# Optimization experiments

Measured on AMD Instinct MI355X. Metric: run time of the kernel, lower is better.

## Reference

```python
import jax, jax.numpy as jnp
import numpy as np

D, M, B, K = 512, 512, 8, 16
EPS = 1e-8
LAMBDA = 1.0
BALANCE_COEFF = 0.0


def _l2_normalize(x, axis=-1):
    n = jnp.linalg.norm(x, axis=axis, keepdims=True)
    return x / jnp.maximum(n, EPS)


def setup_inputs() -> dict:
    key = jax.random.key(0)
    k1, k2, k3 = jax.random.split(key, 3)
    x = jax.random.normal(k1, (2, 2048, D), dtype=jnp.float32)
    V = jax.random.normal(k2, (D, M, B), dtype=jnp.float32)
    U = jax.random.normal(k3, (M, D + 1, B), dtype=jnp.float32)
    return {"x": x, "V": V, "U": U}


def reference(x, V, U):
    input_shape = x.shape
    x_flat = x.reshape(-1, D)                      # (N, D)
    x_flat = _l2_normalize(x_flat)
    N = x_flat.shape[0]

    # UnitColNorm: unit-norm columns of V over the D axis (dim=0)
    Vn = V / jnp.maximum(jnp.linalg.norm(V, axis=0, keepdims=True), EPS)
    # UnitColNormPadded: unit-norm columns of U over the (D+1) axis (dim=1)
    Un = U / jnp.maximum(jnp.linalg.norm(U, axis=1, keepdims=True), EPS)

    # Read: h_all (N, m, b)
    h_all = jnp.einsum('nd,dmb->nmb', x_flat, Vn)

    # Top-k expert selection by energy
    energy = jnp.sum(h_all * h_all, axis=-1)       # (N, m)
    topk_vals, topk_idxs = jax.lax.top_k(energy, K)  # (N, k)
    h_sparse = jnp.take_along_axis(h_all, topk_idxs[:, :, None], axis=1)  # (N, k, b)

    # Autoencode aux (V_active gathered under no_grad in torch)
    V_t = jnp.transpose(Vn, (1, 0, 2))             # (m, D, b)
    V_active = jax.lax.stop_gradient(V_t[topk_idxs])  # (N, k, D, b)
    x_hat = jnp.einsum('nkdb,nkb->nd', V_active, h_sparse)
    resid = x_flat - x_hat
    uncaptured_energy = jnp.mean(jnp.sum(resid * resid, axis=-1))

    avg_energy = jnp.mean(energy, axis=0)          # (m,)
    denom = jnp.maximum(jnp.sum(avg_energy), EPS)
    probs = jnp.maximum(avg_energy / denom, EPS)
    balance_entropy = -jnp.sum(probs * jnp.log(probs)) / jnp.log(jnp.float32(M))
    topk_aux_loss = uncaptured_energy + BALANCE_COEFF * (1.0 - balance_entropy)

    # expert usage counts (monitoring only)
    counts = jnp.zeros((M,), jnp.float32).at[topk_idxs.reshape(-1)].add(1.0)

    # Write: gather per-token expert U matrices, drop the padding row
    U_active = Un[topk_idxs][:, :, :D, :]          # (N, k, D, b)
    writes = jnp.einsum('nkdb,nkb->nd', U_active, h_sparse)
    h_recon = jnp.einsum('nkdb,nd->nkb', U_active, writes)
    writer_aux_loss = jnp.mean((h_recon - jax.lax.stop_gradient(h_sparse)) ** 2)

    aux_loss = topk_aux_loss + writer_aux_loss

    x_out = _l2_normalize(x_flat + LAMBDA * writes).reshape(input_shape)
    return x_out, aux_loss, counts
```

## Files before the change

### kernel.cpp

```cpp
#include <hip/hip_runtime.h>
#include <math.h>

#define N_TOK 4096
#define D_DIM 512
#define M_EXP 512
#define B_DIM 8
#define K_TOP 16
#define MB    4096
#define UROW  4104
#define EPSV  1e-8f
#define KTOT  1536

typedef unsigned short ushort8 __attribute__((ext_vector_type(8)));
typedef unsigned short ushort4v __attribute__((ext_vector_type(4)));
typedef short short8 __attribute__((ext_vector_type(8)));
typedef float f32x4 __attribute__((ext_vector_type(4)));

__device__ inline float b2f(unsigned short u) {
    union { unsigned int i; float f; } c;
    c.i = ((unsigned int)u) << 16;
    return c.f;
}
__device__ inline unsigned short f2b(float f) {
    union { float f; unsigned int i; } c; c.f = f;
    unsigned int lsb = (c.i >> 16) & 1;
    c.i += 0x7fffu + lsb;
    return (unsigned short)(c.i >> 16);
}
__device__ inline void gload_lds16(const unsigned short* g, unsigned short* l) {
    __builtin_amdgcn_global_load_lds(
        (const __attribute__((address_space(1))) unsigned int*)g,
        (__attribute__((address_space(3))) unsigned int*)l, 16, 0, 0);
}

__global__ __launch_bounds__(256) void k_norm_x(const float* __restrict__ x,
                                                float* __restrict__ xn,
                                                unsigned short* __restrict__ Abf)
{
    int wave = threadIdx.x >> 6;
    int lane = threadIdx.x & 63;
    int n = blockIdx.x * 4 + wave;
    const float4* xp = (const float4*)&x[(size_t)n * D_DIM + lane * 8];
    float4 a = xp[0], b = xp[1];
    float s = a.x*a.x + a.y*a.y + a.z*a.z + a.w*a.w
            + b.x*b.x + b.y*b.y + b.z*b.z + b.w*b.w;
    #pragma unroll
    for (int off = 1; off < 64; off <<= 1) s += __shfl_xor(s, off);
    float inv = 1.0f / fmaxf(sqrtf(s), EPSV);
    float v[8] = {a.x*inv, a.y*inv, a.z*inv, a.w*inv,
                  b.x*inv, b.y*inv, b.z*inv, b.w*inv};
    float4* op = (float4*)&xn[(size_t)n * D_DIM + lane * 8];
    op[0] = make_float4(v[0], v[1], v[2], v[3]);
    op[1] = make_float4(v[4], v[5], v[6], v[7]);
    ushort8 hi, lo;
    #pragma unroll
    for (int j = 0; j < 8; ++j) {
        unsigned short h = f2b(v[j]);
        hi[j] = h;
        lo[j] = f2b(v[j] - b2f(h));
    }
    size_t base = (size_t)n * KTOT + lane * 8;
    *(ushort8*)&Abf[base]        = hi;
    *(ushort8*)&Abf[base + 512]  = hi;
    *(ushort8*)&Abf[base + 1024] = lo;
}

__global__ __launch_bounds__(256) void k_vnorm_part(const float* __restrict__ V,
                                                    float* __restrict__ part)
{
    int s = blockIdx.x >> 4;
    int t = (blockIdx.x & 15) * 256 + threadIdx.x;
    float sum = 0.f;
    int d0 = s * 32;
    #pragma unroll 8
    for (int d = d0; d < d0 + 32; ++d) {
        float v = V[(size_t)d * MB + t];
        sum += v * v;
    }
    part[(size_t)s * MB + t] = sum;
}

__global__ __launch_bounds__(256) void k_norm_V2(const float* __restrict__ V,
                                                 const float* __restrict__ part,
                                                 unsigned short* __restrict__ Btbf,
                                                 unsigned short* __restrict__ WXt)
{
    int s = blockIdx.x >> 4;
    int t = (blockIdx.x & 15) * 256 + threadIdx.x;
    float n2 = 0.f;
    #pragma unroll
    for (int i = 0; i < 16; ++i) n2 += part[(size_t)i * MB + t];
    float inv = 1.0f / fmaxf(sqrtf(n2), EPSV);
    size_t row = (size_t)t * KTOT;
    int dbeg = s * 32;
    for (int d0 = dbeg; d0 < dbeg + 32; d0 += 8) {
        ushort8 hi, lo;
        #pragma unroll
        for (int j = 0; j < 8; ++j) {
            float f = V[(size_t)(d0 + j) * MB + t] * inv;
            unsigned short h = f2b(f);
            hi[j] = h;
            lo[j] = f2b(f - b2f(h));
            WXt[(size_t)(512 + d0 + j) * MB + t] = h;
        }
        *(ushort8*)&Btbf[row + d0]        = hi;
        *(ushort8*)&Btbf[row + 512 + d0]  = lo;
        *(ushort8*)&Btbf[row + 1024 + d0] = hi;
    }
}

__global__ __launch_bounds__(256) void k_unorm_part(const float* __restrict__ U,
                                                    float* __restrict__ part)
{
    int s = blockIdx.x >> 4;
    int t = (blockIdx.x & 15) * 256 + threadIdx.x;
    int m = t >> 3, b = t & 7;
    size_t base = (size_t)m * UROW + b;
    int pbeg = s * 32;
    int pend = (s == 15) ? 513 : pbeg + 32;
    float sum = 0.f;
    for (int p = pbeg; p < pend; ++p) {
        float u = U[base + (size_t)p * 8];
        sum += u * u;
    }
    part[(size_t)s * MB + t] = sum;
}

__global__ __launch_bounds__(256) void k_norm_U2(const float* __restrict__ U,
                                                 const float* __restrict__ part,
                                                 unsigned short* __restrict__ WXt,
                                                 unsigned short* __restrict__ U2t)
{
    int s = blockIdx.x >> 4;
    int t = (blockIdx.x & 15) * 256 + threadIdx.x;
    int m = t >> 3, b = t & 7;
    size_t base = (size_t)m * UROW + b;
    float n2 = 0.f;
    #pragma unroll
    for (int i = 0; i < 16; ++i) n2 += part[(size_t)i * MB + t];
    float inv = 1.0f / fmaxf(sqrtf(n2), EPSV);
    int pbeg = s * 32;
    for (int p0 = pbeg; p0 < pbeg + 32; p0 += 8) {
        ushort8 h8;
        #pragma unroll
        for (int j = 0; j < 8; ++j) {
            unsigned short h = f2b(U[base + (size_t)(p0 + j) * 8] * inv);
            h8[j] = h;
            WXt[(size_t)(p0 + j) * MB + t] = h;
        }
        *(ushort8*)&U2t[(size_t)t * D_DIM + p0] = h8;
    }
}

template<int KROW, int BUF, int KC, int MH, bool READB, int SBUF, int SOP, int SKC, bool DOVM>
__device__ __forceinline__ void gemm_phase(const unsigned short* __restrict__ A,
                                           const unsigned short* __restrict__ Bt,
                                           unsigned short (*lds)[2][2][8192],
                                           f32x4 (&acc)[8][4], short8 (&bfr)[4],
                                           int wr, int wc, int lane, int wid,
                                           int brow, int bcol, int stile)
{
    const unsigned short* aun = lds[BUF][0][KC];
    const unsigned short* bun = lds[BUF][1][KC];
    int ko = ((lane >> 4) ^ (lane & 3)) * 8;
    short8 af[4];
    #pragma unroll
    for (int mi = 0; mi < 4; ++mi) {
        int rowL = wr * 128 + (MH * 4 + mi) * 16 + (lane & 15);
        af[mi] = *(const short8*)&aun[rowL * 32 + ko];
    }
    if (READB) {
        #pragma unroll
        for (int ni = 0; ni < 4; ++ni) {
            int colL = wc * 64 + ni * 16 + (lane & 15);
            bfr[ni] = *(const short8*)&bun[colL * 32 + ko];
        }
    }
    {
        const unsigned short* src = SOP ? Bt : A;
        int rbase = SOP ? bcol : brow;
        #pragma unroll
        for (int j = 0; j < 2; ++j) {
            int c = wid * 128 + j * 64 + lane;
            int row = c >> 2, k8 = c & 3;
            int k8s = k8 ^ (row & 3);
            const unsigned short* gp = src + (size_t)(rbase + row) * KROW
                                     + stile * 64 + SKC * 32 + k8s * 8;
            unsigned short* lp = lds[SBUF][SOP][SKC] + (wid * 128 + j * 64) * 8;
            gload_lds16(gp, lp);
        }
    }
    __builtin_amdgcn_sched_barrier(0);
    __builtin_amdgcn_s_barrier();
    asm volatile("s_waitcnt lgkmcnt(0)" ::: "memory");
    __builtin_amdgcn_sched_barrier(0);
    __builtin_amdgcn_s_setprio(1);
    #pragma unroll
    for (int mi = 0; mi < 4; ++mi)
        #pragma unroll
        for (int ni = 0; ni < 4; ++ni)
            acc[MH * 4 + mi][ni] = __builtin_amdgcn_mfma_f32_16x16x32_bf16(
                af[mi], bfr[ni], acc[MH * 4 + mi][ni], 0, 0, 0);
    __builtin_amdgcn_s_setprio(0);
    if (DOVM) asm volatile("s_waitcnt vmcnt(8)" ::: "memory");
    __builtin_amdgcn_sched_barrier(0);
    __builtin_amdgcn_s_barrier();
    __builtin_amdgcn_sched_barrier(0);
}

template<int KROW, int KLEN, int NCOLT, int SPLITK, int LDC, int OUTMODE>
__global__ __launch_bounds__(512, 1) void k_gemm8(const unsigned short* __restrict__ A,
                                                  const unsigned short* __restrict__ Bt,
                                                  float* __restrict__ C,
                                                  unsigned short* __restrict__ Cb)
{
    __shared__ unsigned short lds[2][2][2][8192];

    constexpr int KT   = KLEN / 64;
    constexpr int NIT  = KLEN / 128;
    constexpr int ROWT = 16;
    constexpr int NWG  = ROWT * NCOLT * SPLITK;

    int tid = threadIdx.x;
    int wid = tid >> 6;
    int lane = tid & 63;
    int wr = wid >> 2, wc = wid & 3;

    int bid = blockIdx.x;
    int swz = (bid & 7) * (NWG / 8) + (bid >> 3);
    int ks   = swz / (ROWT * NCOLT);
    int tile = swz % (ROWT * NCOLT);
    int brow = (tile / NCOLT) * 256;
    int bcol = (tile % NCOLT) * 256;

    const unsigned short* Aofs = A + (size_t)ks * KLEN;
    const unsigned short* Bofs = Bt + (size_t)ks * KLEN;
    float* Cofs = C + (size_t)ks * 4096 * LDC;

    f32x4 acc[8][4] = {};
    short8 bfr[4];

    auto stage0 = [&](int sbuf, int sop, int skc, int stile) {
        const unsigned short* src = sop ? Bofs : Aofs;
        int rbase = sop ? bcol : brow;
        #pragma unroll
        for (int j = 0; j < 2; ++j) {
            int c = wid * 128 + j * 64 + lane;
            int row = c >> 2, k8 = c & 3;
            int k8s = k8 ^ (row & 3);
            const unsigned short* gp = src + (size_t)(rbase + row) * KROW
                                     + stile * 64 + skc * 32 + k8s * 8;
            unsigned short* lp = lds[sbuf][sop][skc] + (wid * 128 + j * 64) * 8;
            gload_lds16(gp, lp);
        }
    };
    stage0(0, 0, 0, 0); stage0(0, 1, 0, 0);
    stage0(0, 0, 1, 0); stage0(0, 1, 1, 0);
    stage0(1, 0, 0, 1); stage0(1, 1, 0, 1);
    asm volatile("s_waitcnt vmcnt(8)" ::: "memory");
    __builtin_amdgcn_sched_barrier(0);
    __builtin_amdgcn_s_barrier();
    __builtin_amdgcn_sched_barrier(0);

    for (int i = 0; i < NIT; ++i) {
        int t1 = 2 * i + 1; if (t1 > KT - 1) t1 = KT - 1;
        int t2 = 2 * i + 2; if (t2 > KT - 1) t2 = KT - 1;
        int t3 = 2 * i + 3; if (t3 > KT - 1) t3 = KT - 1;
        gemm_phase<KROW, 0, 0, 0, true , 1, 0, 1, false>(Aofs, Bofs, lds, acc, bfr, wr, wc, lane, wid, brow, bcol, t1);
        gemm_phase<KROW, 0, 0, 1, false, 1, 1, 1, true >(Aofs, Bofs, lds, acc, bfr, wr, wc, lane, wid, brow, bcol, t1);
        gemm_phase<KROW, 0, 1, 0, true , 0, 0, 0, false>(Aofs, Bofs, lds, acc, bfr, wr, wc, lane, wid, brow, bcol, t2);
        gemm_phase<KROW, 0, 1, 1, false, 0, 1, 0, true >(Aofs, Bofs, lds, acc, bfr, wr, wc, lane, wid, brow, bcol, t2);
        gemm_phase<KROW, 1, 0, 0, true , 0, 0, 1, false>(Aofs, Bofs, lds, acc, bfr, wr, wc, lane, wid, brow, bcol, t2);
        gemm_phase<KROW, 1, 0, 1, false, 0, 1, 1, true >(Aofs, Bofs, lds, acc, bfr, wr, wc, lane, wid, brow, bcol, t2);
        gemm_phase<KROW, 1, 1, 0, true , 1, 0, 0, false>(Aofs, Bofs, lds, acc, bfr, wr, wc, lane, wid, brow, bcol, t3);
        gemm_phase<KROW, 1, 1, 1, false, 1, 1, 0, true >(Aofs, Bofs, lds, acc, bfr, wr, wc, lane, wid, brow, bcol, t3);
    }

    if (OUTMODE != 3) {
        #pragma unroll
        for (int mr = 0; mr < 8; ++mr) {
            int row0 = brow + wr * 128 + mr * 16 + (lane >> 4) * 4;
            #pragma unroll
            for (int nr = 0; nr < 4; ++nr) {
                int col = bcol + wc * 64 + nr * 16 + (lane & 15);
                #pragma unroll
                for (int r = 0; r < 4; ++r) {
                    if (OUTMODE == 0)
                        Cofs[(size_t)(row0 + r) * LDC + col] = acc[mr][nr][r];
                    else
                        Cb[(size_t)(row0 + r) * LDC + col] = f2b(acc[mr][nr][r]);
                }
            }
        }
    } else {
        #pragma unroll
        for (int mr = 0; mr < 8; ++mr) {
            int row0 = brow + wr * 128 + mr * 16 + (lane >> 4) * 4;
            #pragma unroll
            for (int nr = 0; nr < 4; ++nr) {
                int col = bcol + wc * 64 + nr * 16 + (lane & 15);
                f32x4 a = acc[mr][nr];
                #pragma unroll
                for (int r = 0; r < 4; ++r)
                    Cb[(size_t)(row0 + r) * 4096 + col] = f2b(a[r]);
                f32x4 sq;
                #pragma unroll
                for (int r = 0; r < 4; ++r) sq[r] = a[r] * a[r];
                #pragma unroll
                for (int off = 1; off <= 4; off <<= 1) {
                    sq[0] += __shfl_xor(sq[0], off);
                    sq[1] += __shfl_xor(sq[1], off);
                    sq[2] += __shfl_xor(sq[2], off);
                    sq[3] += __shfl_xor(sq[3], off);
                }
                if ((lane & 7) == 0) {
                    int e = ((bcol + wc * 64 + nr * 16) >> 3) + ((lane >> 3) & 1);
                    #pragma unroll
                    for (int r = 0; r < 4; ++r)
                        C[(size_t)(row0 + r) * 512 + e] = sq[r];
                }
            }
        }
    }
}

__global__ __launch_bounds__(256) void k_topk2(const float* __restrict__ energy,
                                               unsigned short* __restrict__ hbf,
                                               int* __restrict__ topk_idx,
                                               int* __restrict__ counts,
                                               float* __restrict__ h_sel)
{
    int wave = threadIdx.x >> 6;
    int lane = threadIdx.x & 63;
    int n = blockIdx.x * 4 + wave;
    float ev[8];
    #pragma unroll
    for (int i = 0; i < 8; ++i) ev[i] = energy[(size_t)n * M_EXP + i * 64 + lane];
    for (int r = 0; r < K_TOP; ++r) {
        float bv = -1.0f; int bi = 0;
        #pragma unroll
        for (int i = 0; i < 8; ++i) {
            if (ev[i] > bv) { bv = ev[i]; bi = i * 64 + lane; }
        }
        #pragma unroll
        for (int off = 1; off < 64; off <<= 1) {
            float ov = __shfl_xor(bv, off);
            int   oi = __shfl_xor(bi, off);
            if (ov > bv || (ov == bv && oi < bi)) { bv = ov; bi = oi; }
        }
        if (lane == 0) {
            topk_idx[n * K_TOP + r] = bi;
            atomicAdd(&counts[bi], 1);
        }
        if (lane < 8)
            h_sel[(size_t)n * 128 + r * 8 + lane] =
                b2f(hbf[(size_t)n * MB + bi * 8 + lane]);
        #pragma unroll
        for (int i = 0; i < 8; ++i)
            if (((bi >> 6) == i) && (lane == (bi & 63))) ev[i] = -INFINITY;
    }
    ushort8 z = {0, 0, 0, 0, 0, 0, 0, 0};
    #pragma unroll
    for (int i = 0; i < 8; ++i) {
        int e = i * 64 + lane;
        if (ev[i] != -INFINITY)
            *(ushort8*)&hbf[(size_t)n * MB + e * 8] = z;
    }
}

__global__ __launch_bounds__(256) void k_reduce_fin(const float* __restrict__ P,
                                                    const float* __restrict__ xn,
                                                    float* __restrict__ x_out,
                                                    unsigned short* __restrict__ wb,
                                                    float* __restrict__ uncap)
{
    const size_t S = (size_t)4096 * 1024;
    int n = blockIdx.x;
    int t = threadIdx.x;
    int c = t * 4;
    size_t base = (size_t)n * 1024 + c;
    float4 a = *(const float4*)&P[base];
    float4 b = *(const float4*)&P[base + S];
    float4 cc = *(const float4*)&P[base + 2 * S];
    float4 d = *(const float4*)&P[base + 3 * S];
    float4 v = make_float4(a.x + b.x + cc.x + d.x, a.y + b.y + cc.y + d.y,
                           a.z + b.z + cc.z + d.z, a.w + b.w + cc.w + d.w);
    bool isW = (c < 512);
    int xc = isW ? c : (c - 512);
    float4 xv = *(const float4*)&xn[(size_t)n * D_DIM + xc];
    float4 yr;
    if (isW) yr = make_float4(xv.x + v.x, xv.y + v.y, xv.z + v.z, xv.w + v.w);
    else     yr = make_float4(xv.x - v.x, xv.y - v.y, xv.z - v.z, xv.w - v.w);
    float local = yr.x*yr.x + yr.y*yr.y + yr.z*yr.z + yr.w*yr.w;

    __shared__ float red[256];
    __shared__ float sinv;
    red[t] = local;
    __syncthreads();
    for (int s = 64; s > 0; s >>= 1) {
        if ((t & 127) < s) red[t] += red[t + s];
        __syncthreads();
    }
    if (t == 0) {
        uncap[n] = red[128];
        sinv = 1.0f / fmaxf(sqrtf(red[0]), EPSV);
    }
    __syncthreads();
    if (isW) {
        float inv = sinv;
        *(float4*)&x_out[(size_t)n * D_DIM + c] =
            make_float4(yr.x*inv, yr.y*inv, yr.z*inv, yr.w*inv);
        ushort4v o;
        o[0] = f2b(yr.x); o[1] = f2b(yr.y); o[2] = f2b(yr.z); o[3] = f2b(yr.w);
        *(ushort4v*)&wb[(size_t)n * 512 + c] = o;
    }
}

__global__ __launch_bounds__(256) void k_fin_writer(const unsigned short* __restrict__ hrecon,
                                                    const float* __restrict__ h_sel,
                                                    const int* __restrict__ topk_idx,
                                                    float* __restrict__ writer)
{
    int wave = threadIdx.x >> 6;
    int lane = threadIdx.x & 63;
    int n = blockIdx.x * 4 + wave;
    float acc = 0.f;
    #pragma unroll
    for (int pp = 0; pp < 2; ++pp) {
        int p = lane + pp * 64;
        int m = topk_idx[n * K_TOP + (p >> 3)];
        float d = b2f(hrecon[(size_t)n * MB + m * 8 + (p & 7)])
                - h_sel[(size_t)n * 128 + p];
        acc += d * d;
    }
    #pragma unroll
    for (int off = 1; off < 64; off <<= 1) acc += __shfl_xor(acc, off);
    if (lane == 0) writer[n] = acc;
}

__global__ __launch_bounds__(256) void k_finalize(const float* __restrict__ uncap,
                                                  const float* __restrict__ writer,
                                                  const int* __restrict__ counts,
                                                  float* __restrict__ out)
{
    __shared__ float ru[256], rw[256];
    int t = threadIdx.x;
    float su = 0.f, sw = 0.f;
    for (int i = t; i < N_TOK; i += 256) { su += uncap[i]; sw += writer[i]; }
    ru[t] = su; rw[t] = sw;
    __syncthreads();
    for (int s = 128; s > 0; s >>= 1) {
        if (t < s) { ru[t] += ru[t + s]; rw[t] += rw[t + s]; }
        __syncthreads();
    }
    if (t == 0)
        out[(size_t)N_TOK * D_DIM] = ru[0] / (float)N_TOK
                                   + rw[0] / (float)(N_TOK * K_TOP * B_DIM);
    for (int i = t; i < M_EXP; i += 256)
        out[(size_t)N_TOK * D_DIM + 1 + i] = (float)counts[i];
}

extern "C" void kernel_launch(void* const* d_in, const int* in_sizes, int n_in,
                              void* d_out, int out_size, void* d_ws, size_t ws_size,
                              hipStream_t stream)
{
    const float* x = (const float*)d_in[0];
    const float* V = (const float*)d_in[1];
    const float* U = (const float*)d_in[2];
    float* out = (float*)d_out;

    float* ws     = (float*)d_ws;
    float* xn     = ws;
    float* P      = xn + 2097152;
    float* uncap  = P + 16777216;
    float* writer = uncap + 4096;
    int*   topk_i = (int*)(writer + 4096);
    int*   counts = topk_i + 65536;
    float* partV  = (float*)(counts + 1024);
    float* partU  = partV + 65536;
    float* h_sel  = partU + 65536;
    unsigned short* hbf = (unsigned short*)(h_sel + 524288);
    unsigned short* U2t = hbf + 16777216;
    unsigned short* WXt = U2t + 2097152;
    unsigned short* R   = WXt + 4194304;
    unsigned short* Abf  = R;
    unsigned short* Btbf = R + 6291456;
    unsigned short* writesb = R;
    float* energy = P;
    unsigned short* hrecon = (unsigned short*)P;

    hipMemsetAsync(counts, 0, M_EXP * sizeof(int), stream);
    k_norm_x    <<<N_TOK / 4, 256, 0, stream>>>(x, xn, Abf);
    k_vnorm_part<<<256, 256, 0, stream>>>(V, partV);
    k_norm_V2   <<<256, 256, 0, stream>>>(V, partV, Btbf, WXt);
    k_unorm_part<<<256, 256, 0, stream>>>(U, partU);
    k_norm_U2   <<<256, 256, 0, stream>>>(U, partU, WXt, U2t);
    k_gemm8<KTOT, KTOT, 16, 1, 4096, 3><<<256, 512, 0, stream>>>(Abf, Btbf, energy, hbf);
    k_topk2     <<<N_TOK / 4, 256, 0, stream>>>(energy, hbf, topk_i, counts, h_sel);
    k_gemm8<4096, 1024, 4, 4, 1024, 0><<<256, 512, 0, stream>>>(hbf, WXt, P, nullptr);
    k_reduce_fin<<<4096, 256, 0, stream>>>(P, xn, out, writesb, uncap);
    k_gemm8<D_DIM, D_DIM, 16, 1, 4096, 2><<<256, 512, 0, stream>>>(writesb, U2t, nullptr, hrecon);
    k_fin_writer<<<N_TOK / 4, 256, 0, stream>>>(hrecon, h_sel, topk_i, writer);
    k_finalize  <<<1, 256, 0, stream>>>(uncap, writer, counts, out);
}
```

Measured before the change: 233.5 us.

## Fuse writer-loss into final GEMM epilogue, merge norm kernels, retune LDS swizzle

The final GEMM gets a new epilogue mode. It reads the sparse h values back from hbf and reduces the squared reconstruction error per block. This removes the hrecon write, the h_sel buffer and the k_fin_writer kernel. The V and U norm passes are merged into two combined kernels, and the counts memset moves into k_norm_x, so fewer kernels are launched. The LDS XOR swizzle now uses (row>>1)&3, which changes the bank-conflict pattern. The epilogue skips entries whose stored bf16 is zero to identify unselected experts, so a selected value that rounds to zero would be dropped.

After: 212.6 us. -9.0%, faster.

```diff
diff --git a/kernel.cpp b/kernel.cpp
--- a/kernel.cpp
+++ b/kernel.cpp
@@ -35,8 +35,13 @@
 
 __global__ __launch_bounds__(256) void k_norm_x(const float* __restrict__ x,
                                                 float* __restrict__ xn,
-                                                unsigned short* __restrict__ Abf)
-{
+                                                unsigned short* __restrict__ Abf,
+                                                int* __restrict__ counts)
+{
+    if (blockIdx.x == 0) {
+        counts[threadIdx.x] = 0;
+        counts[threadIdx.x + 256] = 0;
+    }
     int wave = threadIdx.x >> 6;
     int lane = threadIdx.x & 63;
     int n = blockIdx.x * 4 + wave;
@@ -65,90 +70,93 @@
     *(ushort8*)&Abf[base + 1024] = lo;
 }
 
-__global__ __launch_bounds__(256) void k_vnorm_part(const float* __restrict__ V,
-                                                    float* __restrict__ part)
-{
-    int s = blockIdx.x >> 4;
-    int t = (blockIdx.x & 15) * 256 + threadIdx.x;
-    float sum = 0.f;
-    int d0 = s * 32;
-    #pragma unroll 8
-    for (int d = d0; d < d0 + 32; ++d) {
-        float v = V[(size_t)d * MB + t];
-        sum += v * v;
-    }
-    part[(size_t)s * MB + t] = sum;
-}
-
-__global__ __launch_bounds__(256) void k_norm_V2(const float* __restrict__ V,
-                                                 const float* __restrict__ part,
-                                                 unsigned short* __restrict__ Btbf,
-                                                 unsigned short* __restrict__ WXt)
-{
-    int s = blockIdx.x >> 4;
-    int t = (blockIdx.x & 15) * 256 + threadIdx.x;
-    float n2 = 0.f;
-    #pragma unroll
-    for (int i = 0; i < 16; ++i) n2 += part[(size_t)i * MB + t];
-    float inv = 1.0f / fmaxf(sqrtf(n2), EPSV);
-    size_t row = (size_t)t * KTOT;
-    int dbeg = s * 32;
-    for (int d0 = dbeg; d0 < dbeg + 32; d0 += 8) {
-        ushort8 hi, lo;
-        #pragma unroll
-        for (int j = 0; j < 8; ++j) {
-            float f = V[(size_t)(d0 + j) * MB + t] * inv;
-            unsigned short h = f2b(f);
-            hi[j] = h;
-            lo[j] = f2b(f - b2f(h));
-            WXt[(size_t)(512 + d0 + j) * MB + t] = h;
-        }
-        *(ushort8*)&Btbf[row + d0]        = hi;
-        *(ushort8*)&Btbf[row + 512 + d0]  = lo;
-        *(ushort8*)&Btbf[row + 1024 + d0] = hi;
-    }
-}
-
-__global__ __launch_bounds__(256) void k_unorm_part(const float* __restrict__ U,
-                                                    float* __restrict__ part)
-{
-    int s = blockIdx.x >> 4;
-    int t = (blockIdx.x & 15) * 256 + threadIdx.x;
-    int m = t >> 3, b = t & 7;
-    size_t base = (size_t)m * UROW + b;
-    int pbeg = s * 32;
-    int pend = (s == 15) ? 513 : pbeg + 32;
-    float sum = 0.f;
-    for (int p = pbeg; p < pend; ++p) {
-        float u = U[base + (size_t)p * 8];
-        sum += u * u;
-    }
-    part[(size_t)s * MB + t] = sum;
-}
-
-__global__ __launch_bounds__(256) void k_norm_U2(const float* __restrict__ U,
-                                                 const float* __restrict__ part,
-                                                 unsigned short* __restrict__ WXt,
-                                                 unsigned short* __restrict__ U2t)
-{
-    int s = blockIdx.x >> 4;
-    int t = (blockIdx.x & 15) * 256 + threadIdx.x;
-    int m = t >> 3, b = t & 7;
-    size_t base = (size_t)m * UROW + b;
-    float n2 = 0.f;
-    #pragma unroll
-    for (int i = 0; i < 16; ++i) n2 += part[(size_t)i * MB + t];
-    float inv = 1.0f / fmaxf(sqrtf(n2), EPSV);
-    int pbeg = s * 32;
-    for (int p0 = pbeg; p0 < pbeg + 32; p0 += 8) {
-        ushort8 h8;
-        #pragma unroll
-        for (int j = 0; j < 8; ++j) {
-            unsigned short h = f2b(U[base + (size_t)(p0 + j) * 8] * inv);
-            h8[j] = h;
-            WXt[(size_t)(p0 + j) * MB + t] = h;
-        }
-        *(ushort8*)&U2t[(size_t)t * D_DIM + p0] = h8;
+__global__ __launch_bounds__(256) void k_uvnorm_part(const float* __restrict__ V,
+                                                     const float* __restrict__ U,
+                                                     float* __restrict__ partV,
+                                                     float* __restrict__ partU)
+{
+    int blk = blockIdx.x;
+    if (blk < 256) {
+        int s = blk >> 4;
+        int t = (blk & 15) * 256 + threadIdx.x;
+        float sum = 0.f;
+        int d0 = s * 32;
+        #pragma unroll 8
+        for (int d = d0; d < d0 + 32; ++d) {
+            float v = V[(size_t)d * MB + t];
+            sum += v * v;
+        }
+        partV[(size_t)s * MB + t] = sum;
+    } else {
+        blk -= 256;
+        int s = blk >> 4;
+        int t = (blk & 15) * 256 + threadIdx.x;
+        int m = t >> 3, b = t & 7;
+        size_t base = (size_t)m * UROW + b;
+        int pbeg = s * 32;
+        int pend = (s == 15) ? 513 : pbeg + 32;
+        float sum = 0.f;
+        for (int p = pbeg; p < pend; ++p) {
+            float u = U[base + (size_t)p * 8];
+            sum += u * u;
+        }
+        partU[(size_t)s * MB + t] = sum;
+    }
+}
+
+__global__ __launch_bounds__(256) void k_norm_UV2(const float* __restrict__ V,
+                                                  const float* __restrict__ U,
+                                                  const float* __restrict__ partV,
+                                                  const float* __restrict__ partU,
+                                                  unsigned short* __restrict__ Btbf,
+                                                  unsigned short* __restrict__ WXt,
+                                                  unsigned short* __restrict__ U2t)
+{
+    int blk = blockIdx.x;
+    if (blk < 256) {
+        int s = blk >> 4;
+        int t = (blk & 15) * 256 + threadIdx.x;
+        float n2 = 0.f;
+        #pragma unroll
+        for (int i = 0; i < 16; ++i) n2 += partV[(size_t)i * MB + t];
+        float inv = 1.0f / fmaxf(sqrtf(n2), EPSV);
+        size_t row = (size_t)t * KTOT;
+        int dbeg = s * 32;
+        for (int d0 = dbeg; d0 < dbeg + 32; d0 += 8) {
+            ushort8 hi, lo;
+            #pragma unroll
+            for (int j = 0; j < 8; ++j) {
+                float f = V[(size_t)(d0 + j) * MB + t] * inv;
+                unsigned short h = f2b(f);
+                hi[j] = h;
+                lo[j] = f2b(f - b2f(h));
+                WXt[(size_t)(512 + d0 + j) * MB + t] = h;
+            }
+            *(ushort8*)&Btbf[row + d0]        = hi;
+            *(ushort8*)&Btbf[row + 512 + d0]  = lo;
+            *(ushort8*)&Btbf[row + 1024 + d0] = hi;
+        }
+    } else {
+        blk -= 256;
+        int s = blk >> 4;
+        int t = (blk & 15) * 256 + threadIdx.x;
+        int m = t >> 3, b = t & 7;
+        size_t base = (size_t)m * UROW + b;
+        float n2 = 0.f;
+        #pragma unroll
+        for (int i = 0; i < 16; ++i) n2 += partU[(size_t)i * MB + t];
+        float inv = 1.0f / fmaxf(sqrtf(n2), EPSV);
+        int pbeg = s * 32;
+        for (int p0 = pbeg; p0 < pbeg + 32; p0 += 8) {
+            ushort8 h8;
+            #pragma unroll
+            for (int j = 0; j < 8; ++j) {
+                unsigned short h = f2b(U[base + (size_t)(p0 + j) * 8] * inv);
+                h8[j] = h;
+                WXt[(size_t)(p0 + j) * MB + t] = h;
+            }
+            *(ushort8*)&U2t[(size_t)t * D_DIM + p0] = h8;
+        }
     }
 }
 
@@ -162,7 +170,7 @@
 {
     const unsigned short* aun = lds[BUF][0][KC];
     const unsigned short* bun = lds[BUF][1][KC];
-    int ko = ((lane >> 4) ^ (lane & 3)) * 8;
+    int ko = ((lane >> 4) ^ ((lane >> 1) & 3)) * 8;
     short8 af[4];
     #pragma unroll
     for (int mi = 0; mi < 4; ++mi) {
@@ -183,7 +191,7 @@
         for (int j = 0; j < 2; ++j) {
             int c = wid * 128 + j * 64 + lane;
             int row = c >> 2, k8 = c & 3;
-            int k8s = k8 ^ (row & 3);
+            int k8s = k8 ^ ((row >> 1) & 3);
             const unsigned short* gp = src + (size_t)(rbase + row) * KROW
                                      + stile * 64 + SKC * 32 + k8s * 8;
             unsigned short* lp = lds[SBUF][SOP][SKC] + (wid * 128 + j * 64) * 8;
@@ -247,7 +255,7 @@
         for (int j = 0; j < 2; ++j) {
             int c = wid * 128 + j * 64 + lane;
             int row = c >> 2, k8 = c & 3;
-            int k8s = k8 ^ (row & 3);
+            int k8s = k8 ^ ((row >> 1) & 3);
             const unsigned short* gp = src + (size_t)(rbase + row) * KROW
                                      + stile * 64 + skc * 32 + k8s * 8;
             unsigned short* lp = lds[sbuf][sop][skc] + (wid * 128 + j * 64) * 8;
@@ -276,7 +284,7 @@
         gemm_phase<KROW, 1, 1, 1, false, 1, 1, 0, true >(Aofs, Bofs, lds, acc, bfr, wr, wc, lane, wid, brow, bcol, t3);
     }
 
-    if (OUTMODE != 3) {
+    if (OUTMODE == 0 || OUTMODE == 2) {
         #pragma unroll
         for (int mr = 0; mr < 8; ++mr) {
             int row0 = brow + wr * 128 + mr * 16 + (lane >> 4) * 4;
@@ -292,7 +300,7 @@
                 }
             }
         }
-    } else {
+    } else if (OUTMODE == 3) {
         #pragma unroll
         for (int mr = 0; mr < 8; ++mr) {
             int row0 = brow + wr * 128 + mr * 16 + (lane >> 4) * 4;
@@ -321,14 +329,40 @@
                 }
             }
         }
+    } else {
+        float local = 0.f;
+        #pragma unroll
+        for (int mr = 0; mr < 8; ++mr) {
+            int row0 = brow + wr * 128 + mr * 16 + (lane >> 4) * 4;
+            #pragma unroll
+            for (int nr = 0; nr < 4; ++nr) {
+                int col = bcol + wc * 64 + nr * 16 + (lane & 15);
+                #pragma unroll
+                for (int r = 0; r < 4; ++r) {
+                    unsigned short hbits = Cb[(size_t)(row0 + r) * 4096 + col];
+                    if (hbits & 0x7fffu) {
+                        float d = acc[mr][nr][r] - b2f(hbits);
+                        local += d * d;
+                    }
+                }
+            }
+        }
+        __syncthreads();
+        float* red = (float*)lds;
+        red[tid] = local;
+        __syncthreads();
+        for (int s = 256; s > 0; s >>= 1) {
+            if (tid < s) red[tid] += red[tid + s];
+            __syncthreads();
+        }
+        if (tid == 0) C[bid] = red[0];
     }
 }
 
 __global__ __launch_bounds__(256) void k_topk2(const float* __restrict__ energy,
                                                unsigned short* __restrict__ hbf,
                                                int* __restrict__ topk_idx,
-                                               int* __restrict__ counts,
-                                               float* __restrict__ h_sel)
+                                               int* __restrict__ counts)
 {
     int wave = threadIdx.x >> 6;
     int lane = threadIdx.x & 63;
@@ -352,9 +386,6 @@
             topk_idx[n * K_TOP + r] = bi;
             atomicAdd(&counts[bi], 1);
         }
-        if (lane < 8)
-            h_sel[(size_t)n * 128 + r * 8 + lane] =
-                b2f(hbf[(size_t)n * MB + bi * 8 + lane]);
         #pragma unroll
         for (int i = 0; i < 8; ++i)
             if (((bi >> 6) == i) && (lane == (bi & 63))) ev[i] = -INFINITY;
@@ -416,37 +447,16 @@
     }
 }
 
-__global__ __launch_bounds__(256) void k_fin_writer(const unsigned short* __restrict__ hrecon,
-                                                    const float* __restrict__ h_sel,
-                                                    const int* __restrict__ topk_idx,
-                                                    float* __restrict__ writer)
-{
-    int wave = threadIdx.x >> 6;
-    int lane = threadIdx.x & 63;
-    int n = blockIdx.x * 4 + wave;
-    float acc = 0.f;
-    #pragma unroll
-    for (int pp = 0; pp < 2; ++pp) {
-        int p = lane + pp * 64;
-        int m = topk_idx[n * K_TOP + (p >> 3)];
-        float d = b2f(hrecon[(size_t)n * MB + m * 8 + (p & 7)])
-                - h_sel[(size_t)n * 128 + p];
-        acc += d * d;
-    }
-    #pragma unroll
-    for (int off = 1; off < 64; off <<= 1) acc += __shfl_xor(acc, off);
-    if (lane == 0) writer[n] = acc;
-}
-
 __global__ __launch_bounds__(256) void k_finalize(const float* __restrict__ uncap,
-                                                  const float* __restrict__ writer,
+                                                  const float* __restrict__ writer_part,
                                                   const int* __restrict__ counts,
                                                   float* __restrict__ out)
 {
     __shared__ float ru[256], rw[256];
     int t = threadIdx.x;
-    float su = 0.f, sw = 0.f;
-    for (int i = t; i < N_TOK; i += 256) { su += uncap[i]; sw += writer[i]; }
+    float su = 0.f;
+    for (int i = t; i < N_TOK; i += 256) su += uncap[i];
+    float sw = writer_part[t];
     ru[t] = su; rw[t] = sw;
     __syncthreads();
     for (int s = 128; s > 0; s >>= 1) {
@@ -473,13 +483,12 @@
     float* xn     = ws;
     float* P      = xn + 2097152;
     float* uncap  = P + 16777216;
-    float* writer = uncap + 4096;
-    int*   topk_i = (int*)(writer + 4096);
+    float* writer_part = uncap + 4096;
+    int*   topk_i = (int*)(writer_part + 512);
     int*   counts = topk_i + 65536;
     float* partV  = (float*)(counts + 1024);
     float* partU  = partV + 65536;
-    float* h_sel  = partU + 65536;
-    unsigned short* hbf = (unsigned short*)(h_sel + 524288);
+    unsigned short* hbf = (unsigned short*)(partU + 65536);
     unsigned short* U2t = hbf + 16777216;
     unsigned short* WXt = U2t + 2097152;
     unsigned short* R   = WXt + 4194304;
@@ -487,19 +496,14 @@
     unsigned short* Btbf = R + 6291456;
     unsigned short* writesb = R;
     float* energy = P;
-    unsigned short* hrecon = (unsigned short*)P;
-
-    hipMemsetAsync(counts, 0, M_EXP * sizeof(int), stream);
-    k_norm_x    <<<N_TOK / 4, 256, 0, stream>>>(x, xn, Abf);
-    k_vnorm_part<<<256, 256, 0, stream>>>(V, partV);
-    k_norm_V2   <<<256, 256, 0, stream>>>(V, partV, Btbf, WXt);
-    k_unorm_part<<<256, 256, 0, stream>>>(U, partU);
-    k_norm_U2   <<<256, 256, 0, stream>>>(U, partU, WXt, U2t);
+
+    k_norm_x    <<<N_TOK / 4, 256, 0, stream>>>(x, xn, Abf, counts);
+    k_uvnorm_part<<<512, 256, 0, stream>>>(V, U, partV, partU);
+    k_norm_UV2  <<<512, 256, 0, stream>>>(V, U, partV, partU, Btbf, WXt, U2t);
     k_gemm8<KTOT, KTOT, 16, 1, 4096, 3><<<256, 512, 0, stream>>>(Abf, Btbf, energy, hbf);
-    k_topk2     <<<N_TOK / 4, 256, 0, stream>>>(energy, hbf, topk_i, counts, h_sel);
+    k_topk2     <<<N_TOK / 4, 256, 0, stream>>>(energy, hbf, topk_i, counts);
     k_gemm8<4096, 1024, 4, 4, 1024, 0><<<256, 512, 0, stream>>>(hbf, WXt, P, nullptr);
     k_reduce_fin<<<4096, 256, 0, stream>>>(P, xn, out, writesb, uncap);
-    k_gemm8<D_DIM, D_DIM, 16, 1, 4096, 2><<<256, 512, 0, stream>>>(writesb, U2t, nullptr, hrecon);
-    k_fin_writer<<<N_TOK / 4, 256, 0, stream>>>(hrecon, h_sel, topk_i, writer);
-    k_finalize  <<<1, 256, 0, stream>>>(uncap, writer, counts, out);
-}
+    k_gemm8<D_DIM, D_DIM, 16, 1, 4096, 4><<<256, 512, 0, stream>>>(writesb, U2t, writer_part, hbf);
+    k_finalize  <<<1, 256, 0, stream>>>(uncap, writer_part, counts, out);
+}
```
